# Kernel tuning notes

Measured on AMD Instinct MI355X. Metric: run time of the kernel, lower is better.

The kernel has to match this reference:

```python
import jax, jax.numpy as jnp
import numpy as np

ALPHA = 0.7
BETA = 0.3
GAMMA = 4.0
SMALL_LESION_WEIGHT = 10.0
SMOOTH = 1e-05
AREA_THRESH = 100  # region.area < 100 -> small lesion


def _label_components(mask):
    """8-connectivity connected-component labeling via min-label flooding.
    mask: [B,H,W] bool. Returns int32 labels in [0, H*W) for foreground,
    H*W (sentinel) for background. Equivalent partitioning to skimage.measure.label."""
    B, H, W = mask.shape
    BIG = H * W
    ids = jnp.arange(BIG, dtype=jnp.int32).reshape(1, H, W)
    lab0 = jnp.where(mask, ids, BIG)

    def neighbor_min(lab):
        p = jnp.pad(lab, ((0, 0), (1, 1), (1, 1)), constant_values=BIG)
        m = lab
        for di in range(3):  # 3x3 window = self + 8-neighbors
            for dj in range(3):
                m = jnp.minimum(m, p[:, di:di + H, dj:dj + W])
        return jnp.where(mask, m, BIG)

    def cond(state):
        return state[1]

    def body(state):
        lab, _ = state
        new = neighbor_min(lab)
        return new, jnp.any(new != lab)

    lab, _ = jax.lax.while_loop(cond, body, (lab0, jnp.array(True)))
    return lab


def _small_lesion_weights(targets):
    """targets: [B,1,H,W] float. Returns [B,1,H,W] weights: small_lesion_weight on
    pixels of connected components with area < AREA_THRESH, else 1.0."""
    t = targets[:, 0]                      # [B,H,W]
    mask = t > 0.5
    B, H, W = mask.shape
    BIG = H * W
    lab = _label_components(mask)          # [B,H,W] int32
    flat_lab = lab.reshape(B, BIG)
    ones = mask.astype(jnp.float32).reshape(B, BIG)
    # per-image component areas; background pixels fall into segment BIG
    areas = jax.vmap(lambda l, o: jax.ops.segment_sum(o, l, num_segments=BIG + 1))(flat_lab, ones)
    pix_area = jnp.take_along_axis(areas, flat_lab, axis=1).reshape(B, H, W)
    small = mask & (pix_area < AREA_THRESH)
    w = jnp.where(small, SMALL_LESION_WEIGHT, 1.0)
    return w[:, None, :, :]


def _bce_with_logits(x, t):
    # numerically stable elementwise BCE-with-logits
    return jnp.maximum(x, 0.0) - x * t + jnp.log1p(jnp.exp(-jnp.abs(x)))


def setup_inputs() -> dict:
    key = jax.random.key(0)
    k1, k2 = jax.random.split(key)
    B, C, H, W = 8, 1, 1024, 1024
    predictions = jax.random.normal(k1, (B, C, H, W), dtype=jnp.float32)
    targets = (jax.random.uniform(k2, (B, C, H, W)) < 0.05).astype(jnp.float32)
    return {"predictions": predictions, "targets": targets}


def reference(predictions, targets):
    p = jax.nn.sigmoid(predictions)

    # dice loss (global)
    inter = jnp.sum(p * targets)
    union = jnp.sum(p) + jnp.sum(targets)
    dice_loss = 1.0 - (2.0 * inter + SMOOTH) / (union + SMOOTH)

    # focal loss from logits
    bce = _bce_with_logits(predictions, targets)
    is_pos = targets == 1
    p_t = jnp.where(is_pos, p, 1.0 - p)
    alpha_t = jnp.where(is_pos, ALPHA, 1.0 - ALPHA)
    focal_loss = jnp.mean(alpha_t * (1.0 - p_t) ** GAMMA * bce)

    # tversky loss (FN-focused)
    TP = inter
    FP = jnp.sum((1.0 - targets) * p)
    FN = jnp.sum(targets * (1.0 - p))
    tversky_loss = 1.0 - (TP + SMOOTH) / (TP + ALPHA * FP + BETA * FN + SMOOTH)

    # small-lesion weighted BCE (weights are a non-diff function of targets)
    w = _small_lesion_weights(jax.lax.stop_gradient(targets))
    small_lesion_loss = jnp.mean(w * bce)

    return (dice_loss + focal_loss + tversky_loss + small_lesion_loss) / 4.0
```

## Files before the change

kernel.cpp:

```cpp
#include <hip/hip_runtime.h>

typedef unsigned int u32;
typedef unsigned long long u64;

static constexpr int Bb = 8, Hh = 1024, Ww = 1024;
static constexpr int HW     = Hh * Ww;
static constexpr int NPIX   = Bb * HW;
static constexpr int NWORDS = NPIX / 64;
static constexpr int WPR    = Ww / 64;
static constexpr int WPI    = HW / 64;
static constexpr int FNT = 512, FBG = 512;
static constexpr int SWORDS = NWORDS / FBG;
static constexpr int SPX    = SWORDS * 64;
static constexpr int CAP    = 2048;

static constexpr u32 POISON  = 0xAAAAAAAAu;
static constexpr u32 FLAGVAL = 0xC0FFEE00u;
static constexpr u32 LBITS  = 0x3FFFu;
static constexpr u32 BIGF   = 1u << 29;
static constexpr u32 CROSSF = 1u << 30;

__device__ inline u32 lab_load(u32* L, u32 i) {
    return __hip_atomic_load(&L[i], __ATOMIC_RELAXED, __HIP_MEMORY_SCOPE_AGENT);
}
__device__ inline void lab_store(u32* L, u32 i, u32 v) {
    __hip_atomic_store(&L[i], v, __ATOMIC_RELAXED, __HIP_MEMORY_SCOPE_AGENT);
}
__device__ inline u32 find_root(u32* L, u32 x) {
    while (true) {
        u32 p = lab_load(L, x);
        if (p >= (u32)NPIX || p == x) return x;
        x = p;
    }
}
__device__ inline void union_labels(u32* L, u32 a, u32 b) {
    while (true) {
        a = find_root(L, a);
        b = find_root(L, b);
        if (a == b) return;
        if (a < b) { u32 t = a; a = b; b = t; }
        u32 old = atomicMin(&L[a], b);
        if (old == a || old >= (u32)NPIX) return;
        a = old;
    }
}
__device__ inline u64 b_load(const u64* p) {
    return __hip_atomic_load(p, __ATOMIC_RELAXED, __HIP_MEMORY_SCOPE_AGENT);
}
__device__ inline void b_store(u64* p, u64 v) {
    __hip_atomic_store(p, v, __ATOMIC_RELAXED, __HIP_MEMORY_SCOPE_AGENT);
}
__device__ inline double d_load(const double* p) {
    return __hip_atomic_load(p, __ATOMIC_RELAXED, __HIP_MEMORY_SCOPE_AGENT);
}
__device__ inline void d_store(double* p, double v) {
    __hip_atomic_store(p, v, __ATOMIC_RELAXED, __HIP_MEMORY_SCOPE_AGENT);
}

__device__ inline u32 lds_load(u32* L, u32 x) {
    return __hip_atomic_load(&L[x], __ATOMIC_RELAXED, __HIP_MEMORY_SCOPE_WORKGROUP);
}
__device__ inline void lds_store(u32* L, u32 x, u32 v) {
    __hip_atomic_store(&L[x], v, __ATOMIC_RELAXED, __HIP_MEMORY_SCOPE_WORKGROUP);
}
__device__ inline u32 lfind2(u32* L, u32 x) {
    while (true) { u32 p = lds_load(L, x) & LBITS; if (p == x) return x; x = p; }
}
__device__ inline void lunion(u32* L, u32 a, u32 b) {
    while (true) {
        a = lfind2(L, a);
        b = lfind2(L, b);
        if (a == b) return;
        if (a < b) { u32 t = a; a = b; b = t; }
        u32 old = atomicMin(&L[a], b);
        if (old == a) return;
        a = old;
    }
}

__device__ inline double block_reduce(double v, double* lds) {
    for (int o = 32; o > 0; o >>= 1) v += __shfl_down(v, o, 64);
    int wave = threadIdx.x >> 6, lane = threadIdx.x & 63;
    __syncthreads();
    if (lane == 0) lds[wave] = v;
    __syncthreads();
    double r = 0.0;
    if (threadIdx.x == 0)
        for (int w = 0; w < (int)(blockDim.x >> 6); ++w) r += lds[w];
    return r;
}

__device__ inline float bce_pos(float x) {
    return fmaxf(-x, 0.0f) + __logf(1.0f + __expf(-fabsf(x)));
}

__device__ inline u64 spread4(u64 x) {
    x &= 0xFFFFull;
    x = (x | (x << 24)) & 0x000000FF000000FFull;
    x = (x | (x << 12)) & 0x000F000F000F000Full;
    x = (x | (x << 6))  & 0x0303030303030303ull;
    x = (x | (x << 3))  & 0x1111111111111111ull;
    return x;
}

__device__ inline void grid_barrier(u32* ctr, u32* flag) {
    __syncthreads();
    if (threadIdx.x == 0) {
        u32 old = __hip_atomic_fetch_add(ctr, 1u, __ATOMIC_RELAXED,
                                         __HIP_MEMORY_SCOPE_AGENT);
        if (old == POISON + (u32)FBG - 1u) {
            __hip_atomic_store(flag, FLAGVAL, __ATOMIC_RELAXED,
                               __HIP_MEMORY_SCOPE_AGENT);
        } else {
            while (__hip_atomic_load(flag, __ATOMIC_RELAXED,
                                     __HIP_MEMORY_SCOPE_AGENT) == POISON)
                __builtin_amdgcn_s_sleep(8);
        }
    }
    __syncthreads();
}

__device__ inline u64 half_mask(int t) {
    return (t & 1) ? 0xFFFFFFFF00000000ull : 0x00000000FFFFFFFFull;
}

static constexpr int B_CTR0 = 0,  B_FLAG0 = 32, B_CTR1 = 64, B_FLAG1 = 96;
static constexpr int B_CTR2 = 128, B_FLAG2 = 160, B_DONE = 192;

__global__ __launch_bounds__(FNT, 4) void k_all(const float4* __restrict__ pred4,
                                                const float4* __restrict__ targ4,
                                                u32* __restrict__ lab,
                                                u32* __restrict__ area,
                                                double* __restrict__ part,
                                                u64* __restrict__ bnd,
                                                u32* __restrict__ bar,
                                                float* __restrict__ out) {
    extern __shared__ u32 llab[];
    __shared__ u64 smask[SWORDS];
    __shared__ u32 wl[CAP];
    __shared__ u32 wl_n;
    const float* pred = (const float*)pred4;
    double* part_large = part + 6 * FBG;

    const int b    = blockIdx.x;
    const int tid  = threadIdx.x;
    const int lane = tid & 63;
    const int wv   = tid >> 6;
    const int spx  = b * SPX;
    double* rlds   = (double*)llab;

    double d_p = 0, d_t = 0, d_pt = 0, d_f = 0, d_b = 0, d_bf = 0;
    for (int half = 0; half < 2; ++half) {
        float s_p = 0.f, s_t = 0.f, s_pt = 0.f, s_f = 0.f, s_b = 0.f, s_bf = 0.f;
        float4 pv[4], tv[4];
        #pragma unroll
        for (int c = 0; c < 4; ++c) {
            const int chunk = (b * 8 + wv) * 8 + half * 4 + c;
            pv[c] = pred4[chunk * 64 + lane];
            tv[c] = targ4[chunk * 64 + lane];
        }
        #pragma unroll
        for (int c = 0; c < 4; ++c) {
            const int chunk = (b * 8 + wv) * 8 + half * 4 + c;
            const float* xa = &pv[c].x;
            const float* ta = &tv[c].x;
            u32 nib = 0;
            #pragma unroll
            for (int e = 0; e < 4; ++e) {
                const float x = xa[e], t = ta[e];
                const float ee  = __expf(-fabsf(x));
                const float rin = __builtin_amdgcn_rcpf(1.0f + ee);
                const float p   = (x >= 0.0f) ? rin : 1.0f - rin;
                const float bce = fmaxf(x, 0.0f) - x * t + __logf(1.0f + ee);
                const bool  pos = t > 0.5f;
                const float q1  = pos ? (1.0f - p) : p;
                const float at  = pos ? 0.7f : 0.3f;
                const float q2  = q1 * q1;
                s_p  += p;
                s_t  += t;
                s_pt += pos ? p : 0.0f;
                s_f  += at * q2 * q2 * bce;
                s_b  += bce;
                s_bf += pos ? bce : 0.0f;
                if (pos) nib |= 1u << e;
            }
            const u64 B0 = __ballot(nib & 1u);
            const u64 B1 = __ballot(nib & 2u);
            const u64 B2 = __ballot(nib & 4u);
            const u64 B3 = __ballot(nib & 8u);
            const int k = lane & 3;
            const u64 W = spread4(B0 >> (16 * k)) | (spread4(B1 >> (16 * k)) << 1)
                        | (spread4(B2 >> (16 * k)) << 2) | (spread4(B3 >> (16 * k)) << 3);
            if (lane < 4) {
                const int lw  = (chunk << 2) + k - b * SWORDS;
                smask[lw] = W;
                const int ris = lw >> 4, wx = lw & 15;
                if (ris == 0)  b_store(&bnd[b * 32 + wx], W);
                if (ris == 15) b_store(&bnd[b * 32 + 16 + wx], W);
            }
        }
        d_p += s_p; d_t += s_t; d_pt += s_pt; d_f += s_f; d_b += s_b; d_bf += s_bf;
    }
    double r;
    r = block_reduce(d_p,  rlds); if (tid == 0) d_store(&part[0 * FBG + b], r);
    r = block_reduce(d_t,  rlds); if (tid == 0) d_store(&part[1 * FBG + b], r);
    r = block_reduce(d_pt, rlds); if (tid == 0) d_store(&part[2 * FBG + b], r);
    r = block_reduce(d_f,  rlds); if (tid == 0) d_store(&part[3 * FBG + b], r);
    r = block_reduce(d_b,  rlds); if (tid == 0) d_store(&part[4 * FBG + b], r);
    r = block_reduce(d_bf, rlds); if (tid == 0) d_store(&part[5 * FBG + b], r);
    if (tid == 0) wl_n = 0;
    grid_barrier(bar + B_CTR0, bar + B_FLAG0);

    const int lwi   = tid >> 1;
    const u64 hm    = half_mask(tid);
    const u64 cur   = smask[lwi];
    const int lbase = lwi << 6;

    u64 nonIso = 0, nL = 0, nU = 0, nUL = 0, nUR = 0, nDany = 0;
    if (cur & hm) {
        const int ris = lwi >> 4, wx = lwi & 15;
        const int sb  = b & 63;
        u64 lf = wx > 0  ? smask[lwi - 1] : 0;
        u64 rt = wx < 15 ? smask[lwi + 1] : 0;
        u64 up = 0, ul = 0, ur = 0, dn = 0, dl = 0, dr = 0;
        if (ris > 0) {
            up = smask[lwi - 16];
            ul = wx > 0  ? smask[lwi - 17] : 0;
            ur = wx < 15 ? smask[lwi - 15] : 0;
        } else if (sb > 0) {
            const u64* brow = bnd + (b - 1) * 32 + 16;
            up = b_load(brow + wx);
            ul = wx > 0  ? b_load(brow + wx - 1) : 0;
            ur = wx < 15 ? b_load(brow + wx + 1) : 0;
        }
        if (ris < 15) {
            dn = smask[lwi + 16];
            dl = wx > 0  ? smask[lwi + 15] : 0;
            dr = wx < 15 ? smask[lwi + 17] : 0;
        } else if (sb < 63) {
            const u64* brow = bnd + (b + 1) * 32;
            dn = b_load(brow + wx);
            dl = wx > 0  ? b_load(brow + wx - 1) : 0;
            dr = wx < 15 ? b_load(brow + wx + 1) : 0;
        }
        nL = (cur << 1) | (lf >> 63);
        const u64 nR  = (cur >> 1) | (rt << 63);
        nU  = up;
        nUL = (up << 1) | (ul >> 63);
        nUR = (up >> 1) | (ur << 63);
        const u64 nD  = dn;
        const u64 nDL = (dn << 1) | (dl >> 63);
        const u64 nDR = (dn >> 1) | (dr << 63);
        nDany = nD | nDL | nDR;
        nonIso = cur & (nL | nR | nU | nUL | nUR | nDany) & hm;
    }
    __syncthreads();

    {
        int cnt = __builtin_popcountll(nonIso);
        if (cnt) {
            u32 slot = atomicAdd(&wl_n, (u32)cnt);
            u64 w = nonIso;
            while (w) {
                int bb = __builtin_ctzll(w); w &= w - 1;
                const u32 li = (u32)(lbase + bb);
                llab[li] = li;
                if (slot < (u32)CAP) {
                    const u32 f = (u32)((nL  >> bb) & 1)
                                | ((u32)((nU  >> bb) & 1) << 1)
                                | ((u32)((nUL >> bb) & 1) << 2)
                                | ((u32)((nUR >> bb) & 1) << 3)
                                | ((u32)((nDany >> bb) & 1) << 4);
                    wl[slot] = (li << 5) | f;
                }
                ++slot;
            }
        }
    }
    __syncthreads();
    const bool fb  = wl_n > (u32)CAP;
    const u32 nwl  = fb ? 0u : wl_n;

    if (!fb) {
        for (u32 e = tid; e < nwl; e += FNT) {
            const u32 ent = wl[e], li = ent >> 5, f = ent & 31u;
            const u32 ris = li >> 10;
            if (f & 1u) lunion(llab, li, li - 1);
            if (ris > 0) {
                if (f & 2u) lunion(llab, li, li - 1024);
                else {
                    if (f & 4u) lunion(llab, li, li - 1025);
                    if (f & 8u) lunion(llab, li, li - 1023);
                }
            }
        }
        __syncthreads();
        for (u32 e = tid; e < nwl; e += FNT) {
            const u32 ent = wl[e], li = ent >> 5, f = ent & 31u;
            const u32 ris = li >> 10;
            const u32 rr = lfind2(llab, li);
            if (rr != li) lds_store(llab, li, rr);
            atomicAdd(&llab[rr], 1u << 14);
            const u32 gi = (u32)spx + li;
            if (ris == 0 && (f & (2u | 4u | 8u))) {
                atomicOr(&llab[rr], CROSSF);
                const u32 gr = (u32)spx + rr;
                if (f & 2u) union_labels(lab, gr, gi - Ww);
                if (f & 4u) union_labels(lab, gr, gi - Ww - 1);
                if (f & 8u) union_labels(lab, gr, gi - Ww + 1);
            }
            if (ris == 15 && (f & 16u)) {
                atomicOr(&llab[rr], CROSSF);
                union_labels(lab, gi, (u32)spx + rr);
            }
        }
    } else {
        u64 w = cur & (nL | nU | nUL | nUR) & hm;
        while (w) {
            int bb = __builtin_ctzll(w); w &= w - 1;
            const u64 bit = 1ull << bb;
            const u32 gi = (u32)(spx + lbase + bb);
            if (nL & bit) union_labels(lab, gi, gi - 1);
            if (nU & bit) union_labels(lab, gi, gi - Ww);
            else {
                if (nUL & bit) union_labels(lab, gi, gi - Ww - 1);
                if (nUR & bit) union_labels(lab, gi, gi - Ww + 1);
            }
        }
    }
    grid_barrier(bar + B_CTR1, bar + B_FLAG1);

    if (!fb) {
        for (u32 e = tid; e < nwl; e += FNT) {
            const u32 li = wl[e] >> 5;
            const u32 ent = lds_load(llab, li);
            if ((ent & LBITS) != li) continue;
            if (ent & CROSSF) {
                const u32 gr = find_root(lab, (u32)spx + li);
                lab_store(lab, (u32)spx + li, gr);
                atomicAdd(&area[gr], (ent >> 14) & 0x7FFFu);
            } else if (((ent >> 14) & 0x7FFFu) >= 100u) {
                atomicOr(&llab[li], BIGF);
            }
        }
    } else {
        u64 w = nonIso;
        while (w) {
            int bb = __builtin_ctzll(w); w &= w - 1;
            const u32 gi = (u32)(spx + lbase + bb);
            const u32 rr = find_root(lab, gi);
            lab_store(lab, gi, rr);
            atomicAdd(&area[rr], 1u);
        }
    }
    grid_barrier(bar + B_CTR2, bar + B_FLAG2);

    float s = 0.f;
    if (!fb) {
        for (u32 e = tid; e < nwl; e += FNT) {
            const u32 li = wl[e] >> 5;
            const u32 ent = lds_load(llab, li);
            if ((ent & LBITS) == li && (ent & CROSSF)) {
                const u32 gr  = lab_load(lab, (u32)spx + li);
                const u32 tot = __hip_atomic_load(&area[gr], __ATOMIC_RELAXED,
                                                  __HIP_MEMORY_SCOPE_AGENT) - POISON;
                if (tot >= 100u) atomicOr(&llab[li], BIGF);
            }
        }
        __syncthreads();
        for (u32 e = tid; e < nwl; e += FNT) {
            const u32 li = wl[e] >> 5;
            const u32 ent = lds_load(llab, li);
            const u32 rr = ent & LBITS;
            const u32 fl = (rr == li) ? ent : lds_load(llab, rr);
            if (fl & BIGF) s += bce_pos(pred[spx + li]);
        }
    } else {
        u64 w = nonIso;
        while (w) {
            int bb = __builtin_ctzll(w); w &= w - 1;
            const u32 gi = (u32)(spx + lbase + bb);
            const u32 rr = lab_load(lab, gi);
            const u32 cnt = __hip_atomic_load(&area[rr], __ATOMIC_RELAXED,
                                              __HIP_MEMORY_SCOPE_AGENT) - POISON;
            if (cnt >= 100u) s += bce_pos(pred[gi]);
        }
    }
    __syncthreads();
    int* lastFlagP = (int*)&llab[32];

    double rr2 = block_reduce((double)s, rlds);
    if (tid == 0) {
        d_store(&part_large[b], rr2);
        asm volatile("s_waitcnt vmcnt(0)" ::: "memory");
        u32 old = __hip_atomic_fetch_add(bar + B_DONE, 1u, __ATOMIC_RELAXED,
                                         __HIP_MEMORY_SCOPE_AGENT);
        *lastFlagP = (old == POISON + (u32)FBG - 1u);
    }
    __syncthreads();
    if (!*lastFlagP) return;

    double sv[7] = {0, 0, 0, 0, 0, 0, 0};
    for (int j = tid; j < FBG; j += FNT) {
        #pragma unroll
        for (int k = 0; k < 6; ++k) sv[k] += d_load(&part[k * FBG + j]);
        sv[6] += d_load(&part_large[j]);
    }
    double red[7];
    #pragma unroll
    for (int k = 0; k < 7; ++k) red[k] = block_reduce(sv[k], rlds);
    if (tid == 0) {
        double sum_p = red[0], sum_t = red[1], inter = red[2];
        double sum_f = red[3], sum_b = red[4], sum_bf = red[5], large_b = red[6];
        double small_b = sum_bf - large_b;
        double N = (double)NPIX;
        double dice    = 1.0 - (2.0 * inter + 1e-5) / (sum_p + sum_t + 1e-5);
        double focal   = sum_f / N;
        double FP = sum_p - inter, FN = sum_t - inter;
        double tversky = 1.0 - (inter + 1e-5) / (inter + 0.7 * FP + 0.3 * FN + 1e-5);
        double small   = (sum_b + 9.0 * small_b) / N;
        out[0] = (float)((dice + focal + tversky + small) * 0.25);
    }
}

extern "C" void kernel_launch(void* const* d_in, const int* in_sizes, int n_in,
                              void* d_out, int out_size, void* d_ws, size_t ws_size,
                              hipStream_t stream) {
    const float* pred = (const float*)d_in[0];
    const float* targ = (const float*)d_in[1];
    float* out = (float*)d_out;

    char* ws = (char*)d_ws;
    double* part = (double*)ws;
    u64* bnd  = (u64*)(ws + (size_t)(7 * FBG) * sizeof(double));
    u32* lab  = (u32*)(bnd + (size_t)FBG * 32);
    u32* area = lab + NPIX;
    u32* bar  = area + NPIX;

    k_all<<<FBG, FNT, (size_t)SPX * sizeof(u32), stream>>>(
        (const float4*)pred, (const float4*)targ, lab, area, part, bnd, bar, out);
}
```

Baseline: 132.7 us.

## Drop first grid barrier by recomputing halo rows locally; accumulate partials atomically

Each block now builds its top and bottom neighbour boundary bitmasks directly from the targets tensor in shared memory. Previously it read them from a global buffer that other blocks wrote before a grid-wide barrier, so that first grid barrier is removed. Per-block partial sums are accumulated with double atomicAdd into a small accumulator instead of per-block slots, which replaces the last block's reduction with a few loads. All eight input chunks are also loaded up front. The cost is some redundant halo reads and atomic contention. The atomic sums also depend on the workspace's poisoned initial value being negligible as a double.

```diff
diff --git a/kernel.cpp b/kernel.cpp
--- a/kernel.cpp
+++ b/kernel.cpp
@@ -7,8 +7,6 @@
 static constexpr int HW     = Hh * Ww;
 static constexpr int NPIX   = Bb * HW;
 static constexpr int NWORDS = NPIX / 64;
-static constexpr int WPR    = Ww / 64;
-static constexpr int WPI    = HW / 64;
 static constexpr int FNT = 512, FBG = 512;
 static constexpr int SWORDS = NWORDS / FBG;
 static constexpr int SPX    = SWORDS * 64;
@@ -44,17 +42,8 @@
         a = old;
     }
 }
-__device__ inline u64 b_load(const u64* p) {
-    return __hip_atomic_load(p, __ATOMIC_RELAXED, __HIP_MEMORY_SCOPE_AGENT);
-}
-__device__ inline void b_store(u64* p, u64 v) {
-    __hip_atomic_store(p, v, __ATOMIC_RELAXED, __HIP_MEMORY_SCOPE_AGENT);
-}
 __device__ inline double d_load(const double* p) {
     return __hip_atomic_load(p, __ATOMIC_RELAXED, __HIP_MEMORY_SCOPE_AGENT);
-}
-__device__ inline void d_store(double* p, double v) {
-    __hip_atomic_store(p, v, __ATOMIC_RELAXED, __HIP_MEMORY_SCOPE_AGENT);
 }
 
 __device__ inline u32 lds_load(u32* L, u32 x) {
@@ -124,44 +113,44 @@
     return (t & 1) ? 0xFFFFFFFF00000000ull : 0x00000000FFFFFFFFull;
 }
 
-static constexpr int B_CTR0 = 0,  B_FLAG0 = 32, B_CTR1 = 64, B_FLAG1 = 96;
-static constexpr int B_CTR2 = 128, B_FLAG2 = 160, B_DONE = 192;
+static constexpr int B_CTR1 = 0, B_FLAG1 = 32, B_CTR2 = 64, B_FLAG2 = 96, B_DONE = 128;
 
 __global__ __launch_bounds__(FNT, 4) void k_all(const float4* __restrict__ pred4,
                                                 const float4* __restrict__ targ4,
                                                 u32* __restrict__ lab,
                                                 u32* __restrict__ area,
-                                                double* __restrict__ part,
-                                                u64* __restrict__ bnd,
+                                                double* __restrict__ acc,
                                                 u32* __restrict__ bar,
                                                 float* __restrict__ out) {
     extern __shared__ u32 llab[];
     __shared__ u64 smask[SWORDS];
+    __shared__ u64 bndU[16], bndD[16];
     __shared__ u32 wl[CAP];
     __shared__ u32 wl_n;
     const float* pred = (const float*)pred4;
-    double* part_large = part + 6 * FBG;
 
     const int b    = blockIdx.x;
     const int tid  = threadIdx.x;
     const int lane = tid & 63;
     const int wv   = tid >> 6;
     const int spx  = b * SPX;
+    const int sb   = b & 63;
     double* rlds   = (double*)llab;
 
+    float4 pv[8], tv[8];
+    #pragma unroll
+    for (int c = 0; c < 8; ++c) {
+        const int chunk = (b * 8 + wv) * 8 + c;
+        pv[c] = pred4[chunk * 64 + lane];
+        tv[c] = targ4[chunk * 64 + lane];
+    }
     double d_p = 0, d_t = 0, d_pt = 0, d_f = 0, d_b = 0, d_bf = 0;
     for (int half = 0; half < 2; ++half) {
         float s_p = 0.f, s_t = 0.f, s_pt = 0.f, s_f = 0.f, s_b = 0.f, s_bf = 0.f;
-        float4 pv[4], tv[4];
         #pragma unroll
-        for (int c = 0; c < 4; ++c) {
-            const int chunk = (b * 8 + wv) * 8 + half * 4 + c;
-            pv[c] = pred4[chunk * 64 + lane];
-            tv[c] = targ4[chunk * 64 + lane];
-        }
-        #pragma unroll
-        for (int c = 0; c < 4; ++c) {
-            const int chunk = (b * 8 + wv) * 8 + half * 4 + c;
+        for (int cc = 0; cc < 4; ++cc) {
+            const int c = half * 4 + cc;
+            const int chunk = (b * 8 + wv) * 8 + c;
             const float* xa = &pv[c].x;
             const float* ta = &tv[c].x;
             u32 nib = 0;
@@ -191,25 +180,48 @@
             const int k = lane & 3;
             const u64 W = spread4(B0 >> (16 * k)) | (spread4(B1 >> (16 * k)) << 1)
                         | (spread4(B2 >> (16 * k)) << 2) | (spread4(B3 >> (16 * k)) << 3);
-            if (lane < 4) {
-                const int lw  = (chunk << 2) + k - b * SWORDS;
-                smask[lw] = W;
-                const int ris = lw >> 4, wx = lw & 15;
-                if (ris == 0)  b_store(&bnd[b * 32 + wx], W);
-                if (ris == 15) b_store(&bnd[b * 32 + 16 + wx], W);
-            }
+            if (lane < 4) smask[(chunk << 2) + k - b * SWORDS] = W;
         }
         d_p += s_p; d_t += s_t; d_pt += s_pt; d_f += s_f; d_b += s_b; d_bf += s_bf;
     }
     double r;
-    r = block_reduce(d_p,  rlds); if (tid == 0) d_store(&part[0 * FBG + b], r);
-    r = block_reduce(d_t,  rlds); if (tid == 0) d_store(&part[1 * FBG + b], r);
-    r = block_reduce(d_pt, rlds); if (tid == 0) d_store(&part[2 * FBG + b], r);
-    r = block_reduce(d_f,  rlds); if (tid == 0) d_store(&part[3 * FBG + b], r);
-    r = block_reduce(d_b,  rlds); if (tid == 0) d_store(&part[4 * FBG + b], r);
-    r = block_reduce(d_bf, rlds); if (tid == 0) d_store(&part[5 * FBG + b], r);
+    r = block_reduce(d_p,  rlds); if (tid == 0) atomicAdd(&acc[0 * 16], r);
+    r = block_reduce(d_t,  rlds); if (tid == 0) atomicAdd(&acc[1 * 16], r);
+    r = block_reduce(d_pt, rlds); if (tid == 0) atomicAdd(&acc[2 * 16], r);
+    r = block_reduce(d_f,  rlds); if (tid == 0) atomicAdd(&acc[3 * 16], r);
+    r = block_reduce(d_b,  rlds); if (tid == 0) atomicAdd(&acc[4 * 16], r);
+    r = block_reduce(d_bf, rlds); if (tid == 0) atomicAdd(&acc[5 * 16], r);
     if (tid == 0) wl_n = 0;
-    grid_barrier(bar + B_CTR0, bar + B_FLAG0);
+
+    if (tid < 16) {
+        u64 W = 0;
+        if (sb > 0) {
+            const int base4 = (spx - Ww) / 4 + tid * 16;
+            #pragma unroll
+            for (int j = 0; j < 16; ++j) {
+                const float4 t4 = targ4[base4 + j];
+                u64 nb = (t4.x > 0.5f ? 1u : 0u) | (t4.y > 0.5f ? 2u : 0u)
+                       | (t4.z > 0.5f ? 4u : 0u) | (t4.w > 0.5f ? 8u : 0u);
+                W |= nb << (4 * j);
+            }
+        }
+        bndU[tid] = W;
+    } else if (tid < 32) {
+        const int w = tid - 16;
+        u64 W = 0;
+        if (sb < 63) {
+            const int base4 = (spx + SPX) / 4 + w * 16;
+            #pragma unroll
+            for (int j = 0; j < 16; ++j) {
+                const float4 t4 = targ4[base4 + j];
+                u64 nb = (t4.x > 0.5f ? 1u : 0u) | (t4.y > 0.5f ? 2u : 0u)
+                       | (t4.z > 0.5f ? 4u : 0u) | (t4.w > 0.5f ? 8u : 0u);
+                W |= nb << (4 * j);
+            }
+        }
+        bndD[w] = W;
+    }
+    __syncthreads();
 
     const int lwi   = tid >> 1;
     const u64 hm    = half_mask(tid);
@@ -219,39 +231,33 @@
     u64 nonIso = 0, nL = 0, nU = 0, nUL = 0, nUR = 0, nDany = 0;
     if (cur & hm) {
         const int ris = lwi >> 4, wx = lwi & 15;
-        const int sb  = b & 63;
         u64 lf = wx > 0  ? smask[lwi - 1] : 0;
         u64 rt = wx < 15 ? smask[lwi + 1] : 0;
-        u64 up = 0, ul = 0, ur = 0, dn = 0, dl = 0, dr = 0;
+        u64 up, ul, ur, dn, dl, dr;
         if (ris > 0) {
             up = smask[lwi - 16];
             ul = wx > 0  ? smask[lwi - 17] : 0;
             ur = wx < 15 ? smask[lwi - 15] : 0;
-        } else if (sb > 0) {
-            const u64* brow = bnd + (b - 1) * 32 + 16;
-            up = b_load(brow + wx);
-            ul = wx > 0  ? b_load(brow + wx - 1) : 0;
-            ur = wx < 15 ? b_load(brow + wx + 1) : 0;
+        } else {
+            up = bndU[wx];
+            ul = wx > 0  ? bndU[wx - 1] : 0;
+            ur = wx < 15 ? bndU[wx + 1] : 0;
         }
         if (ris < 15) {
             dn = smask[lwi + 16];
             dl = wx > 0  ? smask[lwi + 15] : 0;
             dr = wx < 15 ? smask[lwi + 17] : 0;
-        } else if (sb < 63) {
-            const u64* brow = bnd + (b + 1) * 32;
-            dn = b_load(brow + wx);
-            dl = wx > 0  ? b_load(brow + wx - 1) : 0;
-            dr = wx < 15 ? b_load(brow + wx + 1) : 0;
+        } else {
+            dn = bndD[wx];
+            dl = wx > 0  ? bndD[wx - 1] : 0;
+            dr = wx < 15 ? bndD[wx + 1] : 0;
         }
         nL = (cur << 1) | (lf >> 63);
         const u64 nR  = (cur >> 1) | (rt << 63);
         nU  = up;
         nUL = (up << 1) | (ul >> 63);
         nUR = (up >> 1) | (ur << 63);
-        const u64 nD  = dn;
-        const u64 nDL = (dn << 1) | (dl >> 63);
-        const u64 nDR = (dn >> 1) | (dr << 63);
-        nDany = nD | nDL | nDR;
+        nDany = dn | ((dn << 1) | (dl >> 63)) | ((dn >> 1) | (dr << 63));
         nonIso = cur & (nL | nR | nU | nUL | nUR | nDany) & hm;
     }
     __syncthreads();
@@ -387,11 +393,11 @@
         }
     }
     __syncthreads();
-    int* lastFlagP = (int*)&llab[32];
+    int* lastFlagP = (int*)&llab[64];
 
     double rr2 = block_reduce((double)s, rlds);
     if (tid == 0) {
-        d_store(&part_large[b], rr2);
+        atomicAdd(&acc[6 * 16], rr2);
         asm volatile("s_waitcnt vmcnt(0)" ::: "memory");
         u32 old = __hip_atomic_fetch_add(bar + B_DONE, 1u, __ATOMIC_RELAXED,
                                          __HIP_MEMORY_SCOPE_AGENT);
@@ -400,18 +406,12 @@
     __syncthreads();
     if (!*lastFlagP) return;
 
-    double sv[7] = {0, 0, 0, 0, 0, 0, 0};
-    for (int j = tid; j < FBG; j += FNT) {
-        #pragma unroll
-        for (int k = 0; k < 6; ++k) sv[k] += d_load(&part[k * FBG + j]);
-        sv[6] += d_load(&part_large[j]);
-    }
-    double red[7];
-    #pragma unroll
-    for (int k = 0; k < 7; ++k) red[k] = block_reduce(sv[k], rlds);
+    double* vals = rlds;
+    if (tid < 7) vals[tid] = d_load(&acc[tid * 16]);
+    __syncthreads();
     if (tid == 0) {
-        double sum_p = red[0], sum_t = red[1], inter = red[2];
-        double sum_f = red[3], sum_b = red[4], sum_bf = red[5], large_b = red[6];
+        double sum_p = vals[0], sum_t = vals[1], inter = vals[2];
+        double sum_f = vals[3], sum_b = vals[4], sum_bf = vals[5], large_b = vals[6];
         double small_b = sum_bf - large_b;
         double N = (double)NPIX;
         double dice    = 1.0 - (2.0 * inter + 1e-5) / (sum_p + sum_t + 1e-5);
@@ -431,12 +431,11 @@
     float* out = (float*)d_out;
 
     char* ws = (char*)d_ws;
-    double* part = (double*)ws;
-    u64* bnd  = (u64*)(ws + (size_t)(7 * FBG) * sizeof(double));
-    u32* lab  = (u32*)(bnd + (size_t)FBG * 32);
+    double* acc = (double*)ws;
+    u32* bar  = (u32*)(ws + 1024);
+    u32* lab  = (u32*)(ws + 2048);
     u32* area = lab + NPIX;
-    u32* bar  = area + NPIX;
 
     k_all<<<FBG, FNT, (size_t)SPX * sizeof(u32), stream>>>(
-        (const float4*)pred, (const float4*)targ, lab, area, part, bnd, bar, out);
-}
+        (const float4*)pred, (const float4*)targ, lab, area, acc, bar, out);
+}
```

Result: slower. 154.2 us (+16.2%).
